# Kernel optimization log

Hardware: AMD Instinct MI355X
Metric: run time of the kernel (lower is better)

## Reference

```python
import jax, jax.numpy as jnp
import numpy as np

# Dims: batch N, in_channels C (>=75 so the 0.25/0.75 channel weighting is active),
# prototypes O, 3x3 kernel, 56x56 feature map.
N, C, H, W = 32, 150, 56, 56
O = 225
KH = KW = 3
K = KH * KW
D = C * K  # unfolded feature dim = 1350
SPLIT = 75  # weight_cdist: channels [:75] weight 0.25, [75:] weight 0.75


def setup_inputs() -> dict:
    key = jax.random.key(0)
    k1, k2 = jax.random.split(key)
    x = jax.random.uniform(k1, (N, C, H, W), dtype=jnp.float32)
    # kaiming_uniform_ on a (O, D) matrix: bound = sqrt(6 / fan_in), fan_in = D
    bound = float(np.sqrt(6.0 / D))
    weight = jax.random.uniform(k2, (O, D), jnp.float32, -bound, bound)
    return {"x": x, "weight": weight}


def reference(x, weight):
    n = x.shape[0]
    # im2col, channel-major feature ordering (c, kh, kw) -- matches torch F.unfold
    patches = jax.lax.conv_general_dilated_patches(
        x, (KH, KW), (1, 1), ((1, 1), (1, 1)))  # (N, C*K, H, W)
    windows = patches.reshape(n, D, H * W).transpose(0, 2, 1)  # (N, L, D)
    # per-channel weights, repeated over the K kernel positions
    w = jnp.where(jnp.arange(C) < SPLIT, 0.25, 0.75).astype(x.dtype)
    wfull = jnp.repeat(w, K)  # (D,)
    # weighted squared distance: sum_d wfull_d * (x_d - p_d)^2
    #   = ||x||_w^2 + ||p||_w^2 - 2 * x . (w * p)   (GEMM form, no NxOxLxD tensor)
    x2 = jnp.einsum('nld,d->nl', windows * windows, wfull)          # (N, L)
    p2 = jnp.einsum('od,d->o', weight * weight, wfull)              # (O,)
    xp = jnp.einsum('nld,od->nlo', windows, weight * wfull)         # (N, L, O)
    d2 = x2[:, :, None] + p2[None, None, :] - 2.0 * xp
    dist = jnp.sqrt(jnp.maximum(d2, 1e-12))  # clamp tiny negative GEMM round-off
    # (N, L, O) -> (N, O, H, W)
    return dist.transpose(0, 2, 1).reshape(n, O, H, W)
```

## Files before the change

kernel.cpp:

```cpp
#include <hip/hip_runtime.h>
#include <hip/hip_bf16.h>

#define N_B   32
#define C_IN  150
#define HH    56
#define WW    56
#define O_P   225
#define D_F   1350
#define SPLIT 75

#define C_PAD 192
#define O_PAD 256
#define PSTRB 208
#define NPLANE 58

#define SW    2540.0f
#define SC_I  (1.0f / 322580.0f)

typedef __attribute__((ext_vector_type(4))) int int4v;
typedef __attribute__((ext_vector_type(4))) float f32x4;
typedef unsigned short ushort_t;
typedef unsigned int uint_t;
typedef unsigned char u8;

#define XT_OFF 0
#define WT_OFF 19267584
#define AO_OFF (WT_OFF + 442368)
#define SQ_OFF (AO_OFF + 1024)

__global__ __launch_bounds__(256) void prep_x(const float* __restrict__ x,
                                              u8* __restrict__ xt,
                                              float* __restrict__ sq) {
  __shared__ float tile[C_IN][WW + 1];
  const int n = blockIdx.y, h = blockIdx.x, tid = threadIdx.x;

  for (int idx = tid; idx < C_IN * WW; idx += 256) {
    int c = idx / WW, w = idx % WW;
    tile[c][w] = x[((n * C_IN + c) * HH + h) * WW + w];
  }
  __syncthreads();

  uint4* xt128 = (uint4*)(xt + (size_t)((n * HH + h) * WW) * C_PAD);
  for (int idx = tid; idx < WW * (C_PAD / 16); idx += 256) {
    int w = idx / (C_PAD / 16), q = idx % (C_PAD / 16), c0 = q * 16;
    uint_t words[4];
#pragma unroll
    for (int wd = 0; wd < 4; ++wd) {
      uint_t acc = 0;
#pragma unroll
      for (int b = 0; b < 4; ++b) {
        int c = c0 + wd * 4 + b;
        int v = -127;
        if (c < C_IN) v = __float2int_rn(tile[c][w] * 254.f) - 127;
        acc |= ((uint_t)(u8)(char)v) << (8 * b);
      }
      words[wd] = acc;
    }
    xt128[idx] = make_uint4(words[0], words[1], words[2], words[3]);
  }

  if (tid < WW) {
    float s = 0.f;
    for (int c = 0; c < C_IN; ++c) {
      float v = tile[c][tid];
      s += ((c < SPLIT) ? 0.25f : 0.75f) * v * v;
    }
    sq[(n * HH + h) * WW + tid] = s;
  }
}

__global__ __launch_bounds__(256) void prep_w(const float* __restrict__ wgt,
                                              u8* __restrict__ wt,
                                              float* __restrict__ ao) {
  const int o = blockIdx.x, tid = threadIdx.x;

  for (int idx = tid; idx < 9 * C_PAD; idx += 256) {
    int t = idx / C_PAD, c = idx % C_PAD;
    int v = 0;
    if (o < O_P && c < C_IN) {
      float wc = (c < SPLIT) ? 0.25f : 0.75f;
      float f = wgt[o * D_F + c * 9 + t] * wc * SW;
      v = __float2int_rn(fminf(fmaxf(f, -127.f), 127.f));
    }
    wt[(size_t)(t * O_PAD + o) * C_PAD + c] = (u8)(char)v;
  }

  float s1 = 0.f, s2 = 0.f;
  if (o < O_P)
    for (int d = tid; d < D_F; d += 256) {
      int c = d / 9;
      float wc = (c < SPLIT) ? 0.25f : 0.75f;
      float f = wgt[o * D_F + d] * wc * SW;
      float wq = (float)__float2int_rn(fminf(fmaxf(f, -127.f), 127.f));
      s1 += wq;
      s2 += wq * wq / wc;
    }
  __shared__ float r1[256], r2[256];
  r1[tid] = s1; r2[tid] = s2;
  __syncthreads();
  for (int off = 128; off > 0; off >>= 1) {
    if (tid < off) { r1[tid] += r1[tid + off]; r2[tid] += r2[tid + off]; }
    __syncthreads();
  }
  if (tid == 0) ao[o] = r2[0] / (SW * SW) - r1[0] / SW;
}

__global__ __launch_bounds__(256, 2) void sfm_main(
    const u8* __restrict__ xt, const u8* __restrict__ wt,
    const float* __restrict__ aog, const float* __restrict__ sqg,
    float* __restrict__ out) {
  __shared__ __align__(16) u8 xtile[4 * NPLANE * PSTRB];
  __shared__ float aos[O_PAD];
  __shared__ float sqs[4][NPLANE];
  __shared__ float x2row[128];

  const int n = blockIdx.y, h0 = blockIdx.x * 2, tid = threadIdx.x;
  const int lane = tid & 63, wv = tid >> 6;

  for (int idx = tid; idx < 4 * WW * 12; idx += 256) {
    int dh = idx / (WW * 12);
    int rem = idx % (WW * 12);
    int w = rem / 12, q = rem % 12;
    int hh = h0 + dh - 1;
    uint4 v = make_uint4(0x81818181u, 0x81818181u, 0x81818181u, 0x81818181u);
    if (hh >= 0 && hh < HH)
      v = *(const uint4*)(xt + ((size_t)((n * HH + hh) * WW + w) * C_PAD + q * 16));
    *(uint4*)(&xtile[(dh * NPLANE + (w + 1)) * PSTRB + q * 16]) = v;
  }
  for (int idx = tid; idx < 96; idx += 256) {
    int dh = idx / 24, r = idx % 24, side = r / 12, q = r % 12;
    int pos = side ? 57 : 0;
    *(uint4*)(&xtile[(dh * NPLANE + pos) * PSTRB + q * 16]) =
        make_uint4(0x81818181u, 0x81818181u, 0x81818181u, 0x81818181u);
  }
  for (int idx = tid; idx < 4 * NPLANE; idx += 256) {
    int dh = idx / NPLANE, col = idx % NPLANE;
    int hh = h0 + dh - 1, w = col - 1;
    float v = 0.f;
    if (hh >= 0 && hh < HH && w >= 0 && w < WW)
      v = sqg[(n * HH + hh) * WW + w];
    sqs[dh][col] = v;
  }
  aos[tid] = (tid < O_P) ? aog[tid] : 0.f;
  __syncthreads();

  if (tid < 128) {
    int r = tid >> 6, w = tid & 63;
    if (w < WW) {
      float s = 0.f;
#pragma unroll
      for (int a = 0; a < 3; ++a)
        s += sqs[r + a][w] + sqs[r + a][w + 1] + sqs[r + a][w + 2];
      x2row[tid] = s;
    }
  }
  __syncthreads();

  const int olo = lane & 15, quad = lane >> 4;
  int4v zero4 = {0, 0, 0, 0};
  int4v acc[4][8];
#pragma unroll
  for (int j = 0; j < 4; ++j)
#pragma unroll
    for (int i = 0; i < 8; ++i) acc[j][i] = zero4;

  for (int t = 0; t < 9; ++t) {
    const int dh = t / 3, dwo = t % 3;
    const u8* afp[4];
#pragma unroll
    for (int j = 0; j < 4; ++j) {
      int o = (wv * 4 + j) * 16 + olo;
      afp[j] = wt + ((size_t)(t * O_PAD + o) * C_PAD + quad * 16);
    }
    const u8* bfp[8];
#pragma unroll
    for (int i = 0; i < 8; ++i) {
      int r = i >> 2, iw = i & 3;
      int pos = min(iw * 16 + olo + dwo, 57);
      bfp[i] = &xtile[((dh + r) * NPLANE + pos) * PSTRB + quad * 16];
    }
#pragma unroll
    for (int kc = 0; kc < 3; ++kc) {
      int4v af[4], bf[8];
#pragma unroll
      for (int j = 0; j < 4; ++j) af[j] = *(const int4v*)(afp[j] + kc * 64);
#pragma unroll
      for (int i = 0; i < 8; ++i) bf[i] = *(const int4v*)(bfp[i] + kc * 64);
#pragma unroll
      for (int j = 0; j < 4; ++j)
#pragma unroll
        for (int i = 0; i < 8; ++i)
          acc[j][i] = __builtin_amdgcn_mfma_i32_16x16x64_i8(af[j], bf[i], acc[j][i], 0, 0, 0);
    }
  }

#pragma unroll
  for (int j = 0; j < 4; ++j) {
    int ob = (wv * 4 + j) * 16 + quad * 4;
#pragma unroll
    for (int i = 0; i < 8; ++i) {
      int r = i >> 2, iw = i & 3;
      int w = iw * 16 + olo;
      if (w >= WW) continue;
      int h = h0 + r;
      float x2v = x2row[r * 64 + w];
#pragma unroll
      for (int rg = 0; rg < 4; ++rg) {
        int o = ob + rg;
        if (o < O_P) {
          float d2 = x2v + aos[o] - SC_I * (float)acc[j][i][rg];
          out[((size_t)(n * O_P + o) * HH + h) * WW + w] = sqrtf(fmaxf(d2, 1e-12f));
        }
      }
    }
  }
}

extern "C" void kernel_launch(void* const* d_in, const int* in_sizes, int n_in,
                              void* d_out, int out_size, void* d_ws, size_t ws_size,
                              hipStream_t stream) {
  const float* x      = (const float*)d_in[0];
  const float* weight = (const float*)d_in[1];
  float* out = (float*)d_out;
  char* ws = (char*)d_ws;

  u8* xt = (u8*)(ws + XT_OFF);
  u8* wt = (u8*)(ws + WT_OFF);
  float* ao = (float*)(ws + AO_OFF);
  float* sq = (float*)(ws + SQ_OFF);

  prep_x<<<dim3(HH, N_B), 256, 0, stream>>>(x, xt, sq);
  prep_w<<<dim3(O_PAD), 256, 0, stream>>>(weight, wt, ao);
  sfm_main<<<dim3(HH / 2, N_B), 256, 0, stream>>>(xt, wt, ao, sq, out);
}
```

Before: 231.0 us.

## Switch to 32x32x32 int8 MFMA with 160-channel padding and pre-swizzled weights

The main kernel moves from 16x16x64 to 32x32x32 int8 MFMA tiles, padding channels to 160 instead of 192 to cut wasted K work. Each block now handles one output row instead of two, runs at higher occupancy, and uses a swizzled block-to-(n,h) mapping. The weights are stored in a per-fragment layout so loads are contiguous. prep_x gains vectorized float4 loads, a padded shared tile and a parallel sum-of-squares reduction. In exchange, each block reloads its halo rows with less reuse and issues more global weight loads.

```diff
diff --git a/kernel.cpp b/kernel.cpp
--- a/kernel.cpp
+++ b/kernel.cpp
@@ -1,5 +1,4 @@
 #include <hip/hip_runtime.h>
-#include <hip/hip_bf16.h>
 
 #define N_B   32
 #define C_IN  150
@@ -9,34 +8,40 @@
 #define D_F   1350
 #define SPLIT 75
 
-#define C_PAD 192
+#define C_PAD 160
 #define O_PAD 256
-#define PSTRB 208
+#define PSTR  176
 #define NPLANE 58
 
 #define SW    2540.0f
 #define SC_I  (1.0f / 322580.0f)
 
 typedef __attribute__((ext_vector_type(4))) int int4v;
-typedef __attribute__((ext_vector_type(4))) float f32x4;
-typedef unsigned short ushort_t;
+typedef __attribute__((ext_vector_type(16))) int i32x16;
+typedef unsigned char u8;
 typedef unsigned int uint_t;
-typedef unsigned char u8;
 
 #define XT_OFF 0
-#define WT_OFF 19267584
-#define AO_OFF (WT_OFF + 442368)
+#define WT_OFF 16056320
+#define AO_OFF (WT_OFF + 368640)
 #define SQ_OFF (AO_OFF + 1024)
+
+#define TIDX(c, w) ((c) * 57 + ((c) >> 4) + (w))
 
 __global__ __launch_bounds__(256) void prep_x(const float* __restrict__ x,
                                               u8* __restrict__ xt,
                                               float* __restrict__ sq) {
-  __shared__ float tile[C_IN][WW + 1];
+  __shared__ float tile[150 * 57 + 9 + 56 + 1];
+  __shared__ float sp[4][WW];
   const int n = blockIdx.y, h = blockIdx.x, tid = threadIdx.x;
 
-  for (int idx = tid; idx < C_IN * WW; idx += 256) {
-    int c = idx / WW, w = idx % WW;
-    tile[c][w] = x[((n * C_IN + c) * HH + h) * WW + w];
+  for (int idx = tid; idx < C_IN * 14; idx += 256) {
+    int c = idx / 14, w4 = (idx % 14) * 4;
+    const float4 v = *(const float4*)(&x[((size_t)(n * C_IN + c) * HH + h) * WW + w4]);
+    tile[TIDX(c, w4 + 0)] = v.x;
+    tile[TIDX(c, w4 + 1)] = v.y;
+    tile[TIDX(c, w4 + 2)] = v.z;
+    tile[TIDX(c, w4 + 3)] = v.w;
   }
   __syncthreads();
 
@@ -46,33 +51,39 @@
     uint_t words[4];
 #pragma unroll
     for (int wd = 0; wd < 4; ++wd) {
-      uint_t acc = 0;
+      uint_t a = 0;
 #pragma unroll
       for (int b = 0; b < 4; ++b) {
         int c = c0 + wd * 4 + b;
         int v = -127;
-        if (c < C_IN) v = __float2int_rn(tile[c][w] * 254.f) - 127;
-        acc |= ((uint_t)(u8)(char)v) << (8 * b);
+        if (c < C_IN) v = __float2int_rn(tile[TIDX(c, w)] * 254.f) - 127;
+        a |= ((uint_t)(u8)(char)v) << (8 * b);
       }
-      words[wd] = acc;
+      words[wd] = a;
     }
     xt128[idx] = make_uint4(words[0], words[1], words[2], words[3]);
   }
 
-  if (tid < WW) {
+  if (tid < 224) {
+    int w = tid >> 2, p = tid & 3;
+    int cb = p * 38, ce = min(cb + 38, C_IN);
     float s = 0.f;
-    for (int c = 0; c < C_IN; ++c) {
-      float v = tile[c][tid];
+    for (int c = cb; c < ce; ++c) {
+      float v = tile[TIDX(c, w)];
       s += ((c < SPLIT) ? 0.25f : 0.75f) * v * v;
     }
-    sq[(n * HH + h) * WW + tid] = s;
-  }
+    sp[p][w] = s;
+  }
+  __syncthreads();
+  if (tid < WW)
+    sq[(n * HH + h) * WW + tid] = sp[0][tid] + sp[1][tid] + sp[2][tid] + sp[3][tid];
 }
 
 __global__ __launch_bounds__(256) void prep_w(const float* __restrict__ wgt,
                                               u8* __restrict__ wt,
                                               float* __restrict__ ao) {
   const int o = blockIdx.x, tid = threadIdx.x;
+  const int ot = o >> 5, ol = o & 31;
 
   for (int idx = tid; idx < 9 * C_PAD; idx += 256) {
     int t = idx / C_PAD, c = idx % C_PAD;
@@ -82,7 +93,8 @@
       float f = wgt[o * D_F + c * 9 + t] * wc * SW;
       v = __float2int_rn(fminf(fmaxf(f, -127.f), 127.f));
     }
-    wt[(size_t)(t * O_PAD + o) * C_PAD + c] = (u8)(char)v;
+    int kc = c >> 5, hi2 = (c >> 4) & 1, b = c & 15;
+    wt[((((size_t)(t * 8 + ot) * 5 + kc) * 2 + hi2) * 32 + ol) * 16 + b] = (u8)(char)v;
   }
 
   float s1 = 0.f, s2 = 0.f;
@@ -105,111 +117,105 @@
   if (tid == 0) ao[o] = r2[0] / (SW * SW) - r1[0] / SW;
 }
 
-__global__ __launch_bounds__(256, 2) void sfm_main(
+__global__ __launch_bounds__(256, 3) void sfm_main(
     const u8* __restrict__ xt, const u8* __restrict__ wt,
     const float* __restrict__ aog, const float* __restrict__ sqg,
     float* __restrict__ out) {
-  __shared__ __align__(16) u8 xtile[4 * NPLANE * PSTRB];
+  __shared__ __align__(16) u8 xtile[3 * NPLANE * PSTR];
   __shared__ float aos[O_PAD];
-  __shared__ float sqs[4][NPLANE];
-  __shared__ float x2row[128];
-
-  const int n = blockIdx.y, h0 = blockIdx.x * 2, tid = threadIdx.x;
-  const int lane = tid & 63, wv = tid >> 6;
-
-  for (int idx = tid; idx < 4 * WW * 12; idx += 256) {
-    int dh = idx / (WW * 12);
-    int rem = idx % (WW * 12);
-    int w = rem / 12, q = rem % 12;
+  __shared__ float sqs[3][NPLANE];
+  __shared__ float x2row[64];
+
+  const int bid0 = blockIdx.y * 56 + blockIdx.x;
+  const int bid = (bid0 & 7) * ((N_B * HH) >> 3) + (bid0 >> 3);
+  const int h0 = bid % HH, n = bid / HH;
+  const int tid = threadIdx.x, lane = tid & 63, wv = tid >> 6;
+  const int l31 = lane & 31, hi = lane >> 5;
+
+  for (int idx = tid; idx < 3 * WW * (C_PAD / 16); idx += 256) {
+    int dh = idx / (WW * 10), rem = idx % (WW * 10);
+    int w = rem / 10, q = rem % 10;
     int hh = h0 + dh - 1;
     uint4 v = make_uint4(0x81818181u, 0x81818181u, 0x81818181u, 0x81818181u);
     if (hh >= 0 && hh < HH)
       v = *(const uint4*)(xt + ((size_t)((n * HH + hh) * WW + w) * C_PAD + q * 16));
-    *(uint4*)(&xtile[(dh * NPLANE + (w + 1)) * PSTRB + q * 16]) = v;
-  }
-  for (int idx = tid; idx < 96; idx += 256) {
-    int dh = idx / 24, r = idx % 24, side = r / 12, q = r % 12;
+    *(uint4*)(&xtile[(dh * NPLANE + (w + 1)) * PSTR + q * 16]) = v;
+  }
+  for (int idx = tid; idx < 60; idx += 256) {
+    int dh = idx / 20, r = idx % 20, side = r / 10, q = r % 10;
     int pos = side ? 57 : 0;
-    *(uint4*)(&xtile[(dh * NPLANE + pos) * PSTRB + q * 16]) =
+    *(uint4*)(&xtile[(dh * NPLANE + pos) * PSTR + q * 16]) =
         make_uint4(0x81818181u, 0x81818181u, 0x81818181u, 0x81818181u);
   }
-  for (int idx = tid; idx < 4 * NPLANE; idx += 256) {
+  for (int idx = tid; idx < 3 * NPLANE; idx += 256) {
     int dh = idx / NPLANE, col = idx % NPLANE;
     int hh = h0 + dh - 1, w = col - 1;
     float v = 0.f;
-    if (hh >= 0 && hh < HH && w >= 0 && w < WW)
-      v = sqg[(n * HH + hh) * WW + w];
+    if (hh >= 0 && hh < HH && w >= 0 && w < WW) v = sqg[(n * HH + hh) * WW + w];
     sqs[dh][col] = v;
   }
   aos[tid] = (tid < O_P) ? aog[tid] : 0.f;
   __syncthreads();
 
-  if (tid < 128) {
-    int r = tid >> 6, w = tid & 63;
-    if (w < WW) {
-      float s = 0.f;
+  if (tid < 64) {
+    float s = 0.f;
+    if (tid < WW) {
 #pragma unroll
       for (int a = 0; a < 3; ++a)
-        s += sqs[r + a][w] + sqs[r + a][w + 1] + sqs[r + a][w + 2];
-      x2row[tid] = s;
-    }
-  }
-  __syncthreads();
-
-  const int olo = lane & 15, quad = lane >> 4;
-  int4v zero4 = {0, 0, 0, 0};
-  int4v acc[4][8];
-#pragma unroll
-  for (int j = 0; j < 4; ++j)
-#pragma unroll
-    for (int i = 0; i < 8; ++i) acc[j][i] = zero4;
-
+        s += sqs[a][tid] + sqs[a][tid + 1] + sqs[a][tid + 2];
+    }
+    x2row[tid] = s;
+  }
+  __syncthreads();
+
+  int vb[2][3];
+#pragma unroll
+  for (int i = 0; i < 2; ++i)
+#pragma unroll
+    for (int d = 0; d < 3; ++d)
+      vb[i][d] = min(i * 32 + l31 + d, 57) * PSTR + hi * 16;
+
+  const u8* ap0 = wt + ((size_t)(wv * 2 + 0) * 5120 + hi * 512 + l31 * 16);
+  const u8* ap1 = wt + ((size_t)(wv * 2 + 1) * 5120 + hi * 512 + l31 * 16);
+
+  const i32x16 z = {0, 0, 0, 0, 0, 0, 0, 0, 0, 0, 0, 0, 0, 0, 0, 0};
+  i32x16 acc[2][2] = {{z, z}, {z, z}};
+
+#pragma unroll
   for (int t = 0; t < 9; ++t) {
     const int dh = t / 3, dwo = t % 3;
-    const u8* afp[4];
-#pragma unroll
-    for (int j = 0; j < 4; ++j) {
-      int o = (wv * 4 + j) * 16 + olo;
-      afp[j] = wt + ((size_t)(t * O_PAD + o) * C_PAD + quad * 16);
-    }
-    const u8* bfp[8];
-#pragma unroll
-    for (int i = 0; i < 8; ++i) {
-      int r = i >> 2, iw = i & 3;
-      int pos = min(iw * 16 + olo + dwo, 57);
-      bfp[i] = &xtile[((dh + r) * NPLANE + pos) * PSTRB + quad * 16];
-    }
-#pragma unroll
-    for (int kc = 0; kc < 3; ++kc) {
-      int4v af[4], bf[8];
-#pragma unroll
-      for (int j = 0; j < 4; ++j) af[j] = *(const int4v*)(afp[j] + kc * 64);
-#pragma unroll
-      for (int i = 0; i < 8; ++i) bf[i] = *(const int4v*)(bfp[i] + kc * 64);
-#pragma unroll
-      for (int j = 0; j < 4; ++j)
-#pragma unroll
-        for (int i = 0; i < 8; ++i)
-          acc[j][i] = __builtin_amdgcn_mfma_i32_16x16x64_i8(af[j], bf[i], acc[j][i], 0, 0, 0);
-    }
-  }
-
-#pragma unroll
-  for (int j = 0; j < 4; ++j) {
-    int ob = (wv * 4 + j) * 16 + quad * 4;
-#pragma unroll
-    for (int i = 0; i < 8; ++i) {
-      int r = i >> 2, iw = i & 3;
-      int w = iw * 16 + olo;
-      if (w >= WW) continue;
-      int h = h0 + r;
-      float x2v = x2row[r * 64 + w];
-#pragma unroll
-      for (int rg = 0; rg < 4; ++rg) {
-        int o = ob + rg;
-        if (o < O_P) {
-          float d2 = x2v + aos[o] - SC_I * (float)acc[j][i][rg];
-          out[((size_t)(n * O_P + o) * HH + h) * WW + w] = sqrtf(fmaxf(d2, 1e-12f));
+    const u8* a0 = ap0 + t * 40960;
+    const u8* a1 = ap1 + t * 40960;
+    const u8* b0 = &xtile[dh * (NPLANE * PSTR) + vb[0][dwo]];
+    const u8* b1 = &xtile[dh * (NPLANE * PSTR) + vb[1][dwo]];
+#pragma unroll
+    for (int kc = 0; kc < 5; ++kc) {
+      int4v af0 = *(const int4v*)(a0 + kc * 1024);
+      int4v af1 = *(const int4v*)(a1 + kc * 1024);
+      int4v bf0 = *(const int4v*)(b0 + kc * 32);
+      int4v bf1 = *(const int4v*)(b1 + kc * 32);
+      acc[0][0] = __builtin_amdgcn_mfma_i32_32x32x32_i8(af0, bf0, acc[0][0], 0, 0, 0);
+      acc[1][0] = __builtin_amdgcn_mfma_i32_32x32x32_i8(af1, bf0, acc[1][0], 0, 0, 0);
+      acc[0][1] = __builtin_amdgcn_mfma_i32_32x32x32_i8(af0, bf1, acc[0][1], 0, 0, 0);
+      acc[1][1] = __builtin_amdgcn_mfma_i32_32x32x32_i8(af1, bf1, acc[1][1], 0, 0, 0);
+    }
+  }
+
+#pragma unroll
+  for (int jo = 0; jo < 2; ++jo) {
+    const int ob = wv * 64 + jo * 32 + hi * 4;
+#pragma unroll
+    for (int ip = 0; ip < 2; ++ip) {
+      const int w = ip * 32 + l31;
+      if (w < WW) {
+        const float x2v = x2row[w];
+#pragma unroll
+        for (int rg = 0; rg < 16; ++rg) {
+          const int o = ob + (rg & 3) + 8 * (rg >> 2);
+          if (o < O_P) {
+            float d2 = x2v + aos[o] - SC_I * (float)acc[jo][ip][rg];
+            out[((size_t)(n * O_P + o) * HH + h0) * WW + w] = sqrtf(fmaxf(d2, 1e-12f));
+          }
         }
       }
     }
@@ -231,5 +237,5 @@
 
   prep_x<<<dim3(HH, N_B), 256, 0, stream>>>(x, xt, sq);
   prep_w<<<dim3(O_PAD), 256, 0, stream>>>(weight, wt, ao);
-  sfm_main<<<dim3(HH / 2, N_B), 256, 0, stream>>>(xt, wt, ao, sq, out);
-}
+  sfm_main<<<dim3(HH, N_B), 256, 0, stream>>>(xt, wt, ao, sq, out);
+}
```

Measured after the change: 213.2 us. -7.7%, faster.
